# Optimization experiments

Hardware: AMD Instinct MI355X
Metric: run time of the kernel (lower is better)

## Reference

```python
import jax, jax.numpy as jnp
import numpy as np

B, S = 8, 512
HIDDEN = 513
SPATIAL = HIDDEN - 1           # 512
F = SPATIAL // 2 + 1           # 257 rfft bins
F2, F4 = 2 * F, 4 * F          # 514, 1028
IN_DIM = F2 + F2 + 2 * SPATIAL # 2052
MAX_STEPS = 20
TOL = 1e-3


def _ln(x, g, b):
    m = x.mean(-1, keepdims=True)
    v = ((x - m) ** 2).mean(-1, keepdims=True)
    return (x - m) * jax.lax.rsqrt(v + 1e-5) * g + b


def _freq_net(x, w1, b1, g, beta, w2, b2):
    # Linear -> LayerNorm -> GELU(exact) -> Linear -> Tanh
    h = jax.nn.gelu(_ln(x @ w1 + b1, g, beta), approximate=False)
    return jnp.tanh(h @ w2 + b2)


def _mlp(x, w1, b1, w2, b2):
    # Linear -> GELU(exact) -> Linear
    return jax.nn.gelu(x @ w1 + b1, approximate=False) @ w2 + b2


def setup_inputs() -> dict:
    key = jax.random.key(0)
    ks = jax.random.split(key, 16)
    def n(k, shape, s=0.05):
        return jax.random.normal(k, shape, jnp.float32) * s
    return dict(
        carrier_in=n(ks[0], (B, S, SPATIAL), 1.0),
        trajectory_in=n(ks[1], (B, S, SPATIAL), 1.0),
        source_pos=n(ks[2], (B, HIDDEN), 1.0),
        target_pos=n(ks[3], (B, HIDDEN), 1.0),
        cw1=n(ks[4], (IN_DIM, F4)), cb1=jnp.zeros(F4), cg=jnp.ones(F4), cbeta=jnp.zeros(F4),
        cw2=n(ks[5], (F4, F2)), cb2=jnp.zeros(F2),
        tw1=n(ks[6], (IN_DIM, F4)), tb1=jnp.zeros(F4), tg=jnp.ones(F4), tbeta=jnp.zeros(F4),
        tw2=n(ks[7], (F4, F2)), tb2=jnp.zeros(F2),
        freq_damping=jnp.linspace(0.95, 0.5, F).astype(jnp.float32),
        dw1=n(ks[8], (F2, F)), db1=jnp.zeros(F), dw2=n(ks[9], (F, 1)), db2=jnp.ones(1),
        sw1=n(ks[10], (F2, F // 2)), sb1=jnp.zeros(F // 2), sw2=n(ks[11], (F // 2, 1)), sb2=jnp.ones(1),
        carrier_scale=jnp.float32(0.1), trajectory_scale=jnp.float32(0.1),
    )


def reference(carrier_in, trajectory_in, source_pos, target_pos,
              cw1, cb1, cg, cbeta, cw2, cb2,
              tw1, tb1, tg, tbeta, tw2, tb2,
              freq_damping, dw1, db1, dw2, db2,
              sw1, sb1, sw2, sb2,
              carrier_scale, trajectory_scale):
    b, s, _ = carrier_in.shape
    src = jnp.broadcast_to(source_pos[:, None, :SPATIAL], (b, s, SPATIAL))
    tgt = jnp.broadcast_to(target_pos[:, None, :SPATIAL], (b, s, SPATIAL))

    def to_flat(x):  # rfft -> view_as_real -> flatten: [b,s,2F] (re,im interleaved)
        f = jnp.fft.rfft(x, axis=-1)
        return jnp.stack([f.real, f.imag], axis=-1).reshape(b, s, F2).astype(jnp.float32)

    c0 = to_flat(carrier_in)
    t0 = to_flat(trajectory_in)
    # torch: repeat(1,1,2).flatten -> tiled [d_0..d_{F-1}, d_0..d_{F-1}]
    damping = jnp.concatenate([freq_damping, freq_damping])

    def clamp10(x):
        nrm = jnp.linalg.norm(x)
        return jnp.where(nrm > 10.0, x * (10.0 / nrm), x)

    def step(carry, _):
        c, t, done = carry
        combined = jnp.concatenate([c, t, src, tgt], axis=-1)  # [b,s,IN_DIM]
        fc = _freq_net(combined, cw1, cb1, cg, cbeta, cw2, cb2)
        ft = _freq_net(combined, tw1, tb1, tg, tbeta, tw2, tb2)
        safe_c = jnp.nan_to_num(c, nan=0.0, posinf=1e6, neginf=-1e6)
        safe_t = jnp.nan_to_num(t, nan=0.0, posinf=1e6, neginf=-1e6)
        alpha_c = jax.nn.sigmoid(_mlp(safe_c, dw1, db1, dw2, db2))
        alpha_t = jax.nn.sigmoid(_mlp(safe_t, dw1, db1, dw2, db2))
        gamma = jax.nn.sigmoid(_mlp(safe_c, sw1, sb1, sw2, sb2)) + 0.5
        alpha_c = jnp.where(jnp.isnan(alpha_c), 0.0, alpha_c)
        alpha_t = jnp.where(jnp.isnan(alpha_t), 0.0, alpha_t)
        new_c = damping * c + gamma * alpha_c * carrier_scale * fc
        new_t = damping * t + gamma * alpha_t * trajectory_scale * ft
        dc = jnp.linalg.norm(new_c - c, axis=-1).mean()
        dt = jnp.linalg.norm(new_t - t, axis=-1).mean()
        conv = (dc < TOL) & (dt < TOL)
        # on convergence the torch loop breaks BEFORE the norm clamp
        out_c = jnp.where(conv, new_c, clamp10(new_c))
        out_t = jnp.where(conv, new_t, clamp10(new_t))
        out_c = jnp.where(done, c, out_c)
        out_t = jnp.where(done, t, out_t)
        return (out_c, out_t, done | conv), None

    (cf, tf, _), _ = jax.lax.scan(step, (c0, t0, jnp.array(False)), None, length=MAX_STEPS)

    def to_spatial(x):
        xr = x.reshape(b, s, F, 2)
        return jnp.fft.irfft(xr[..., 0] + 1j * xr[..., 1], n=SPATIAL, axis=-1).astype(jnp.float32)

    return to_spatial(cf), to_spatial(tf)


if __name__ == '__main__':
    out = reference(**setup_inputs())
    print(out[0].shape, out[1].shape)
```

## Files before the change

### kernel.cpp

```cpp
#include <hip/hip_runtime.h>
#include <hip/hip_bf16.h>
#include <math.h>

typedef __hip_bfloat16 bf16;
using s16x8 = __attribute__((ext_vector_type(8))) short;
using f32x4 = __attribute__((ext_vector_type(4))) float;
typedef __attribute__((address_space(1))) const unsigned int gu32;
typedef __attribute__((address_space(3))) unsigned int lu32;

#define RTOT 4096
#define XCT  1056
#define NT1  2304
#define HLD  2176
#define KH   1088
#define CLD  640
#define KDP  576
#define NDC  512
#define F2E  514
#define SP   512

__device__ __forceinline__ float gelu_ex(float x) {
    return 0.5f * x * (1.0f + erff(x * 0.70710678118654752f));
}
__device__ __forceinline__ float sigm(float x) { return 1.0f / (1.0f + expf(-x)); }
__device__ __forceinline__ float n2n(float x) {
    if (isnan(x)) return 0.0f;
    if (isinf(x)) return x > 0.0f ? 1e6f : -1e6f;
    return x;
}
__device__ __forceinline__ unsigned short bfb(float x) {
    __hip_bfloat16 h = __float2bfloat16(x);
    return *(unsigned short*)&h;
}
__device__ __forceinline__ unsigned packbf(float x, float y) {
    return (unsigned)bfb(x) | ((unsigned)bfb(y) << 16);
}
__device__ __forceinline__ void glds16(const bf16* g, short* l) {
    __builtin_amdgcn_global_load_lds((gu32*)g, (lu32*)l, 16, 0, 0);
}

template<int EPI>
__global__ __launch_bounds__(256)
void gemm_bt(const bf16* __restrict__ A, int lda,
             const bf16* __restrict__ Bt, int ldb,
             float* __restrict__ C, int ldc,
             const float* __restrict__ bias, int bias_ld, int ktiles,
             long zA, long zB, long zC, long zBias)
{
    A    += (long)blockIdx.z * zA;
    Bt   += (long)blockIdx.z * zB;
    C    += (long)blockIdx.z * zC;
    bias += (long)blockIdx.z * zBias;

    __shared__ __align__(16) short As[128 * 32];
    __shared__ __align__(16) short Bs[128 * 32];
    const int tid  = threadIdx.x;
    const int lane = tid & 63;
    const int wave = tid >> 6;
    const int l15  = lane & 15, kl = lane >> 4;
    const long mb = (long)blockIdx.x * 128;
    const long nb = (long)blockIdx.y * 128;
    const int wr = (wave >> 1) * 64;
    const int wc = (wave & 1) * 64;

    f32x4 acc[4][4] = {};

    const int grp_r = lane >> 2;
    const int gcol  = (lane & 3) * 8;
    const bf16* gA0 = A  + (mb + wave * 32 + grp_r) * (long)lda + gcol;
    const bf16* gA1 = gA0 + 16 * (long)lda;
    const bf16* gB0 = Bt + (nb + wave * 32 + grp_r) * (long)ldb + gcol;
    const bf16* gB1 = gB0 + 16 * (long)ldb;
    short* lA0 = &As[(wave * 32) * 32];
    short* lA1 = &As[(wave * 32 + 16) * 32];
    short* lB0 = &Bs[(wave * 32) * 32];
    short* lB1 = &Bs[(wave * 32 + 16) * 32];

    for (int kt = 0; kt < ktiles; ++kt) {
        const long ko = (long)kt * 32;
        __syncthreads();
        glds16(gA0 + ko, lA0);
        glds16(gA1 + ko, lA1);
        glds16(gB0 + ko, lB0);
        glds16(gB1 + ko, lB1);
        __syncthreads();
        s16x8 af[4], bfr[4];
#pragma unroll
        for (int m = 0; m < 4; ++m) {
            int ar = wr + m * 16 + l15;
            af[m] = *reinterpret_cast<const s16x8*>(&As[ar * 32 + kl * 8]);
        }
#pragma unroll
        for (int n = 0; n < 4; ++n) {
            int br = wc + n * 16 + l15;
            bfr[n] = *reinterpret_cast<const s16x8*>(&Bs[br * 32 + kl * 8]);
        }
#pragma unroll
        for (int m = 0; m < 4; ++m)
#pragma unroll
            for (int n = 0; n < 4; ++n)
                acc[m][n] = __builtin_amdgcn_mfma_f32_16x16x32_bf16(af[m], bfr[n], acc[m][n], 0, 0, 0);
    }

    const float* brow = bias + (bias_ld ? (long)(mb >> 9) * bias_ld : 0);
#pragma unroll
    for (int m = 0; m < 4; ++m) {
        const long grow0 = mb + wr + m * 16 + kl * 4;
#pragma unroll
        for (int n = 0; n < 4; ++n) {
            const long gcol2 = nb + wc + n * 16 + l15;
            const float bb = brow[gcol2];
            f32x4 v = acc[m][n];
#pragma unroll
            for (int r = 0; r < 4; ++r) {
                float x = v[r] + bb;
                if (EPI == 1) x = tanhf(x);
                else if (EPI == 2) x = gelu_ex(x);
                C[(grow0 + r) * (long)ldc + gcol2] = x;
            }
        }
    }
}

__global__ __launch_bounds__(256)
void sgemm_bt(const float* __restrict__ A, int lda,
              const float* __restrict__ Bt, int ldb,
              float* __restrict__ C, int ldc, int ktiles)
{
    __shared__ float As[16][68];
    __shared__ float Bs[16][68];
    const int tid = threadIdx.x;
    const int tx = tid & 15, ty = tid >> 4;
    const int lr = tid >> 2, lc = (tid & 3) * 4;
    const long mb = (long)blockIdx.x * 64, nb = (long)blockIdx.y * 64;
    float acc[4][4] = {};
    const float* Ap = A  + (mb + lr) * (long)lda + lc;
    const float* Bp = Bt + (nb + lr) * (long)ldb + lc;
    for (int kt = 0; kt < ktiles; ++kt) {
        float4 av = *(const float4*)(Ap + kt * 16);
        float4 bv = *(const float4*)(Bp + kt * 16);
        __syncthreads();
        As[lc + 0][lr] = av.x; As[lc + 1][lr] = av.y;
        As[lc + 2][lr] = av.z; As[lc + 3][lr] = av.w;
        Bs[lc + 0][lr] = bv.x; Bs[lc + 1][lr] = bv.y;
        Bs[lc + 2][lr] = bv.z; Bs[lc + 3][lr] = bv.w;
        __syncthreads();
#pragma unroll
        for (int kk = 0; kk < 16; ++kk) {
            float4 a = *(const float4*)&As[kk][ty * 4];
            float4 b = *(const float4*)&Bs[kk][tx * 4];
            acc[0][0] = fmaf(a.x, b.x, acc[0][0]); acc[0][1] = fmaf(a.x, b.y, acc[0][1]);
            acc[0][2] = fmaf(a.x, b.z, acc[0][2]); acc[0][3] = fmaf(a.x, b.w, acc[0][3]);
            acc[1][0] = fmaf(a.y, b.x, acc[1][0]); acc[1][1] = fmaf(a.y, b.y, acc[1][1]);
            acc[1][2] = fmaf(a.y, b.z, acc[1][2]); acc[1][3] = fmaf(a.y, b.w, acc[1][3]);
            acc[2][0] = fmaf(a.z, b.x, acc[2][0]); acc[2][1] = fmaf(a.z, b.y, acc[2][1]);
            acc[2][2] = fmaf(a.z, b.z, acc[2][2]); acc[2][3] = fmaf(a.z, b.w, acc[2][3]);
            acc[3][0] = fmaf(a.w, b.x, acc[3][0]); acc[3][1] = fmaf(a.w, b.y, acc[3][1]);
            acc[3][2] = fmaf(a.w, b.z, acc[3][2]); acc[3][3] = fmaf(a.w, b.w, acc[3][3]);
        }
    }
#pragma unroll
    for (int i = 0; i < 4; ++i) {
        float4 st = { acc[i][0], acc[i][1], acc[i][2], acc[i][3] };
        *(float4*)&C[(mb + ty * 4 + i) * (long)ldc + nb + tx * 4] = st;
    }
}

__global__ void build_tables(float* __restrict__ RT, float* __restrict__ IT)
{
    long idx = (long)blockIdx.x * 256 + threadIdx.x;
    const double W = 6.283185307179586476925286766559005768 / 512.0;
    if (idx < 640L * 512) {
        int r = (int)(idx >> 9), n = (int)(idx & 511);
        float v = 0.f;
        if (r < F2E) {
            int bin = r >> 1;
            int m = (bin * n) & 511;
            double ang = W * m;
            v = (r & 1) ? (float)(-sin(ang)) : (float)cos(ang);
        }
        RT[idx] = v;
    } else {
        long j2 = idx - 640L * 512;
        if (j2 < 512L * 640) {
            int n = (int)(j2 / 640), j = (int)(j2 % 640);
            float v = 0.f;
            if (j < F2E) {
                int bin = j >> 1;
                int m = (bin * n) & 511;
                double ang = W * m;
                bool edge = (bin == 0 || bin == 256);
                double ck = edge ? 1.0 : 2.0;
                if (j & 1) v = edge ? 0.f : (float)(-ck * sin(ang) / 512.0);
                else       v = (float)(ck * cos(ang) / 512.0);
            }
            IT[j2] = v;
        }
    }
}

__global__ void build_damp(float* damp, const float* __restrict__ fd)
{
    int i = blockIdx.x * 256 + threadIdx.x;
    if (i < F2E) damp[i] = fd[i < 257 ? i : i - 257];
}

__global__ void ybase_build(const float* __restrict__ srcp, const float* __restrict__ tgtp,
                            const float* __restrict__ cw1, const float* __restrict__ cb1,
                            const float* __restrict__ tw1, const float* __restrict__ tb1,
                            float* __restrict__ Yb)
{
    const int b = blockIdx.x;
    const int n = blockIdx.y * 256 + threadIdx.x;
    if (n >= NT1) return;
    float acc = 0.f;
    const bool isT = n >= 1152;
    const int nn = isT ? n - 1152 : n;
    if (nn < 1028) {
        const float* w  = isT ? tw1 : cw1;
        acc = (isT ? tb1 : cb1)[nn];
        const float* wst = w + (size_t)1028 * 1028 + nn;
        const float* wtg = w + (size_t)1540 * 1028 + nn;
        const float* s = srcp + b * 513;
        const float* t = tgtp + b * 513;
        for (int k = 0; k < 512; ++k) {
            acc = fmaf(s[k], wst[(size_t)k * 1028], acc);
            acc = fmaf(t[k], wtg[(size_t)k * 1028], acc);
        }
    }
    Yb[b * NT1 + n] = acc;
}

__global__ void wprep(bf16* __restrict__ dst, int ldk,
                      const float* s0, int K0, int N0, int r00,
                      const float* s1, int K1, int N1, int r01)
{
    int r = blockIdx.x;
    int k = blockIdx.y * 256 + threadIdx.x;
    if (k >= ldk) return;
    float v = 0.f;
    if (s0 && r >= r00 && r < r00 + N0 && k < K0) v = s0[(long)k * N0 + (r - r00)];
    if (s1 && r >= r01 && r < r01 + N1 && k < K1) v = s1[(long)k * N1 + (r - r01)];
    dst[(long)r * ldk + k] = __float2bfloat16(v);
}

__global__ void bias_fill(float* __restrict__ dst, int n,
                          const float* s0, int l0, int o0,
                          const float* s1, int l1, int o1)
{
    int i = blockIdx.x * 256 + threadIdx.x;
    if (i >= n) return;
    float v = 0.f;
    if (s0 && i >= o0 && i < o0 + l0) v = s0[i - o0];
    if (s1 && i >= o1 && i < o1 + l1) v = s1[i - o1];
    dst[i] = v;
}

__global__ void initconv(const float* __restrict__ cb, const float* __restrict__ tb,
                         bf16* __restrict__ X, bf16* __restrict__ Cb, bf16* __restrict__ Tb)
{
    int row = blockIdx.x;
    for (int j = threadIdx.x; j < F2E; j += 256) {
        float cv = cb[(long)row * CLD + j], tv = tb[(long)row * CLD + j];
        X[(long)row * XCT + j]        = __float2bfloat16(cv);
        X[(long)row * XCT + 514 + j]  = __float2bfloat16(tv);
        Cb[(long)row * KDP + j] = __float2bfloat16(n2n(cv));
        Tb[(long)row * KDP + j] = __float2bfloat16(n2n(tv));
    }
}

__global__ void xpad_zero(bf16* __restrict__ X)
{
    int row = blockIdx.x;
    int j = 1028 + threadIdx.x;
    if (j < XCT) X[(long)row * XCT + j] = __float2bfloat16(0.f);
}

__global__ __launch_bounds__(256)
void ln_gelu(const float* __restrict__ Y, bf16* __restrict__ H,
             const float* __restrict__ cg, const float* __restrict__ cbeta,
             const float* __restrict__ tg, const float* __restrict__ tbeta)
{
    const int lane = threadIdx.x & 63, wave = threadIdx.x >> 6;
    const int p = blockIdx.x * 4 + wave;
    const int row = p >> 1, net = p & 1;
    const float4* y4 = (const float4*)(Y + (long)row * NT1 + net * 1152);
    float4 v[4], vt = {0.f, 0.f, 0.f, 0.f};
    float s = 0.f;
#pragma unroll
    for (int k = 0; k < 4; ++k) {
        v[k] = y4[lane + k * 64];
        s += v[k].x + v[k].y + v[k].z + v[k].w;
    }
    if (lane == 0) { vt = y4[256]; s += vt.x + vt.y + vt.z + vt.w; }
#pragma unroll
    for (int o = 1; o < 64; o <<= 1) s += __shfl_xor(s, o, 64);
    const float mean = s * (1.0f / 1028.0f);
    float vs = 0.f;
#pragma unroll
    for (int k = 0; k < 4; ++k) {
        float a = v[k].x - mean, b = v[k].y - mean, c = v[k].z - mean, d = v[k].w - mean;
        vs += a * a + b * b + c * c + d * d;
    }
    if (lane == 0) {
        float a = vt.x - mean, b = vt.y - mean, c = vt.z - mean, d = vt.w - mean;
        vs += a * a + b * b + c * c + d * d;
    }
#pragma unroll
    for (int o = 1; o < 64; o <<= 1) vs += __shfl_xor(vs, o, 64);
    const float rs = rsqrtf(vs * (1.0f / 1028.0f) + 1e-5f);
    const float4* g4 = (const float4*)(net ? tg : cg);
    const float4* b4 = (const float4*)(net ? tbeta : cbeta);
    bf16* h = H + (long)row * HLD + (long)net * KH;
#pragma unroll
    for (int k = 0; k < 4; ++k) {
        int j = lane + k * 64;
        float4 gv = g4[j], bv = b4[j];
        ushort4 o;
        o.x = bfb(gelu_ex((v[k].x - mean) * rs * gv.x + bv.x));
        o.y = bfb(gelu_ex((v[k].y - mean) * rs * gv.y + bv.y));
        o.z = bfb(gelu_ex((v[k].z - mean) * rs * gv.z + bv.z));
        o.w = bfb(gelu_ex((v[k].w - mean) * rs * gv.w + bv.w));
        *(ushort4*)(&h[j * 4]) = o;
    }
    if (lane == 0) {
        float4 gv = g4[256], bv = b4[256];
        ushort4 o;
        o.x = bfb(gelu_ex((vt.x - mean) * rs * gv.x + bv.x));
        o.y = bfb(gelu_ex((vt.y - mean) * rs * gv.y + bv.y));
        o.z = bfb(gelu_ex((vt.z - mean) * rs * gv.z + bv.z));
        o.w = bfb(gelu_ex((vt.w - mean) * rs * gv.w + bv.w));
        *(ushort4*)(&h[1024]) = o;
    }
}

__global__ __launch_bounds__(256)
void fused_update(const float* __restrict__ Hd,
                  const float* __restrict__ dw2, const float* __restrict__ db2,
                  const float* __restrict__ sw2, const float* __restrict__ sb2,
                  const float* __restrict__ c, const float* __restrict__ t,
                  const float* __restrict__ fc, const float* __restrict__ ft,
                  float* __restrict__ nc, float* __restrict__ nt,
                  const float* __restrict__ damp,
                  const float* __restrict__ csc, const float* __restrict__ tsc,
                  float* __restrict__ part)
{
    __shared__ float red[16];
    const int tid = threadIdx.x, lane = tid & 63, wave = tid >> 6;
    const int row = blockIdx.x * 4 + wave;

    const float* hc = Hd + (long)row * NDC;
    const float* ht = Hd + (long)(4096 + row) * NDC;
    float s1 = 0.f, s2 = 0.f, s3 = 0.f;
#pragma unroll
    for (int k = 0; k < 4; ++k) {
        int j = lane + k * 64;
        s1 += hc[j] * dw2[j];
        s3 += ht[j] * dw2[j];
    }
    if (lane == 0) { s1 += hc[256] * dw2[256]; s3 += ht[256] * dw2[256]; }
#pragma unroll
    for (int k = 0; k < 2; ++k) {
        int j = lane + k * 64;
        s2 += hc[257 + j] * sw2[j];
    }
#pragma unroll
    for (int o = 1; o < 64; o <<= 1) {
        s1 += __shfl_xor(s1, o, 64);
        s2 += __shfl_xor(s2, o, 64);
        s3 += __shfl_xor(s3, o, 64);
    }
    float a  = sigm(s1 + db2[0]);
    float at = sigm(s3 + db2[0]);
    float g  = sigm(s2 + sb2[0]) + 0.5f;
    if (isnan(a))  a  = 0.f;
    if (isnan(at)) at = 0.f;
    const float gac = g * a  * csc[0];
    const float gat = g * at * tsc[0];

    const float2* c2  = (const float2*)(c  + (long)row * CLD);
    const float2* t2  = (const float2*)(t  + (long)row * CLD);
    const float2* fc2 = (const float2*)(fc + (long)row * CLD);
    const float2* ft2 = (const float2*)(ft + (long)row * CLD);
    float2* nc2 = (float2*)(nc + (long)row * CLD);
    float2* nt2 = (float2*)(nt + (long)row * CLD);
    const float2* d2 = (const float2*)damp;
    float sdc = 0.f, snc = 0.f, sdt = 0.f, snt = 0.f;
#pragma unroll
    for (int k = 0; k < 4; ++k) {
        int j = lane + k * 64;
        float2 dv = d2[j];
        float2 cv = c2[j], fv = fc2[j];
        float2 ncv = { dv.x * cv.x + gac * fv.x, dv.y * cv.y + gac * fv.y };
        nc2[j] = ncv;
        float dx = ncv.x - cv.x, dy = ncv.y - cv.y;
        sdc += dx * dx + dy * dy;
        snc += ncv.x * ncv.x + ncv.y * ncv.y;
        float2 tv = t2[j], gv = ft2[j];
        float2 ntv = { dv.x * tv.x + gat * gv.x, dv.y * tv.y + gat * gv.y };
        nt2[j] = ntv;
        dx = ntv.x - tv.x; dy = ntv.y - tv.y;
        sdt += dx * dx + dy * dy;
        snt += ntv.x * ntv.x + ntv.y * ntv.y;
    }
    if (lane == 0) {
        float2 dv = d2[256];
        float2 cv = c2[256], fv = fc2[256];
        float2 ncv = { dv.x * cv.x + gac * fv.x, dv.y * cv.y + gac * fv.y };
        nc2[256] = ncv;
        float dx = ncv.x - cv.x, dy = ncv.y - cv.y;
        sdc += dx * dx + dy * dy;
        snc += ncv.x * ncv.x + ncv.y * ncv.y;
        float2 tv = t2[256], gv = ft2[256];
        float2 ntv = { dv.x * tv.x + gat * gv.x, dv.y * tv.y + gat * gv.y };
        nt2[256] = ntv;
        dx = ntv.x - tv.x; dy = ntv.y - tv.y;
        sdt += dx * dx + dy * dy;
        snt += ntv.x * ntv.x + ntv.y * ntv.y;
    }
#pragma unroll
    for (int o = 1; o < 64; o <<= 1) {
        sdc += __shfl_xor(sdc, o, 64);
        snc += __shfl_xor(snc, o, 64);
        sdt += __shfl_xor(sdt, o, 64);
        snt += __shfl_xor(snt, o, 64);
    }
    if (lane == 0) {
        red[wave * 4 + 0] = sqrtf(sdc);
        red[wave * 4 + 1] = sqrtf(sdt);
        red[wave * 4 + 2] = snc;
        red[wave * 4 + 3] = snt;
    }
    __syncthreads();
    if (tid < 4)
        part[tid * 1024 + blockIdx.x] =
            red[0 * 4 + tid] + red[1 * 4 + tid] + red[2 * 4 + tid] + red[3 * 4 + tid];
}

__global__ __launch_bounds__(256)
void update2(const float* __restrict__ part, float* __restrict__ scal, int step)
{
    __shared__ float red[4];
    const int tid = threadIdx.x, lane = tid & 63, wave = tid >> 6;
    const float* pq = part + wave * 1024;
    float s = 0.f;
#pragma unroll
    for (int k = 0; k < 16; ++k) s += pq[lane + k * 64];
#pragma unroll
    for (int o = 1; o < 64; o <<= 1) s += __shfl_xor(s, o, 64);
    if (lane == 0) red[wave] = s;
    __syncthreads();
    if (tid == 0) {
        float dc = red[0] * (1.0f / 4096.0f);
        float dt = red[1] * (1.0f / 4096.0f);
        bool conv = (dc < 1e-3f) && (dt < 1e-3f);
        float done = scal[140];
        scal[120 + step] = (done != 0.f) ? 0.f : 1.f;
        float nrc = sqrtf(red[2]);
        float nrt = sqrtf(red[3]);
        scal[80 + step]  = conv ? 1.f : (nrc > 10.f ? 10.f / nrc : 1.f);
        scal[100 + step] = conv ? 1.f : (nrt > 10.f ? 10.f / nrt : 1.f);
        scal[140] = (done != 0.f || conv) ? 1.f : 0.f;
    }
}

__global__ __launch_bounds__(256)
void update3(float* __restrict__ c, float* __restrict__ t,
             const float* __restrict__ nc, const float* __restrict__ nt,
             bf16* __restrict__ X, bf16* __restrict__ Cb, bf16* __restrict__ Tb,
             const float* __restrict__ scal, int step)
{
    if (scal[120 + step] == 0.f) return;
    const float sc = scal[80 + step], st = scal[100 + step];
    const int lane = threadIdx.x & 63, wave = threadIdx.x >> 6;
    const int row = blockIdx.x * 4 + wave;
    const float2* nc2 = (const float2*)(nc + (long)row * CLD);
    const float2* nt2 = (const float2*)(nt + (long)row * CLD);
    float2* c2 = (float2*)(c + (long)row * CLD);
    float2* t2 = (float2*)(t + (long)row * CLD);
    bf16* xr = X  + (long)row * XCT;
    bf16* cb = Cb + (long)row * KDP;
    bf16* tb = Tb + (long)row * KDP;
#pragma unroll
    for (int k = 0; k < 5; ++k) {
        int j = lane + k * 64;
        if (k == 4 && lane > 0) break;
        float2 cv = nc2[j]; cv.x *= sc; cv.y *= sc;
        float2 tv = nt2[j]; tv.x *= st; tv.y *= st;
        c2[j] = cv;
        t2[j] = tv;
        *(unsigned*)(xr + j * 2)       = packbf(cv.x, cv.y);
        *(unsigned*)(xr + 514 + j * 2) = packbf(tv.x, tv.y);
        *(unsigned*)(cb + j * 2) = packbf(n2n(cv.x), n2n(cv.y));
        *(unsigned*)(tb + j * 2) = packbf(n2n(tv.x), n2n(tv.y));
    }
}

extern "C" void kernel_launch(void* const* d_in, const int* in_sizes, int n_in,
                              void* d_out, int out_size, void* d_ws, size_t ws_size,
                              hipStream_t stream)
{
    (void)in_sizes; (void)n_in; (void)out_size; (void)ws_size;
    const float* carrier = (const float*)d_in[0];
    const float* traj    = (const float*)d_in[1];
    const float* srcp    = (const float*)d_in[2];
    const float* tgtp    = (const float*)d_in[3];
    const float* cw1 = (const float*)d_in[4];  const float* cb1 = (const float*)d_in[5];
    const float* cg  = (const float*)d_in[6];  const float* cbe = (const float*)d_in[7];
    const float* cw2 = (const float*)d_in[8];  const float* cb2 = (const float*)d_in[9];
    const float* tw1 = (const float*)d_in[10]; const float* tb1 = (const float*)d_in[11];
    const float* tg  = (const float*)d_in[12]; const float* tbe = (const float*)d_in[13];
    const float* tw2 = (const float*)d_in[14]; const float* tb2 = (const float*)d_in[15];
    const float* fd  = (const float*)d_in[16];
    const float* dw1 = (const float*)d_in[17]; const float* db1 = (const float*)d_in[18];
    const float* dw2 = (const float*)d_in[19]; const float* db2 = (const float*)d_in[20];
    const float* sw1 = (const float*)d_in[21]; const float* sb1 = (const float*)d_in[22];
    const float* sw2 = (const float*)d_in[23]; const float* sb2 = (const float*)d_in[24];
    const float* csc = (const float*)d_in[25]; const float* tsc = (const float*)d_in[26];

    char* p = (char*)d_ws;
    size_t off = 0;
    auto take = [&](size_t bytes) { size_t o = off; off += (bytes + 255) & ~(size_t)255; return o; };
    bf16*  Xct  = (bf16*) (p + take((size_t)RTOT * XCT * 2));
    bf16*  W1ct = (bf16*) (p + take((size_t)NT1 * XCT * 2));
    float* Y    = (float*)(p + take((size_t)RTOT * NT1 * 4));
    bf16*  H    = (bf16*) (p + take((size_t)RTOT * HLD * 2));
    bf16*  W2t  = (bf16*) (p + take((size_t)1280 * KH * 2));
    bf16*  Wdc  = (bf16*) (p + take((size_t)NDC * KDP * 2));
    float* Ybase= (float*)(p + take((size_t)8 * NT1 * 4));
    float* b2c  = (float*)(p + take(1280 * 4));
    float* bdc  = (float*)(p + take(NDC * 4));
    float* RT   = (float*)(p + take(640L * 512 * 4));
    float* IT   = (float*)(p + take(512L * 640 * 4));
    float* damp = (float*)(p + take(F2E * 4));
    float* cbuf = (float*)(p + take((size_t)RTOT * CLD * 4));
    float* tbuf = (float*)(p + take((size_t)RTOT * CLD * 4));
    float* ncb  = (float*)(p + take((size_t)RTOT * CLD * 4));
    float* ntb  = (float*)(p + take((size_t)RTOT * CLD * 4));
    float* fcb  = (float*)(p + take((size_t)2 * RTOT * CLD * 4));
    float* ftb  = fcb + (size_t)RTOT * CLD;
    bf16*  Cbb  = (bf16*) (p + take((size_t)2 * RTOT * KDP * 2));
    bf16*  Tbb  = Cbb + (size_t)RTOT * KDP;
    float* Hd   = (float*)(p + take((size_t)2 * RTOT * NDC * 4));
    float* part = (float*)(p + take(4096 * 4));
    float* scal = (float*)(p + take(1024));

    hipMemsetAsync(scal, 0, 1024, stream);

    build_tables<<<2560, 256, 0, stream>>>(RT, IT);
    build_damp<<<3, 256, 0, stream>>>(damp, fd);
    ybase_build<<<dim3(8, 9), 256, 0, stream>>>(srcp, tgtp, cw1, cb1, tw1, tb1, Ybase);
    wprep<<<dim3(NT1, 5), 256, 0, stream>>>(W1ct, XCT, cw1, 1028, 1028, 0, tw1, 1028, 1028, 1152);
    wprep<<<dim3(1280, 5), 256, 0, stream>>>(W2t, KH, cw2, 1028, 514, 0, tw2, 1028, 514, 640);
    wprep<<<dim3(NDC, 3), 256, 0, stream>>>(Wdc, KDP, dw1, 514, 257, 0, sw1, 514, 128, 257);
    bias_fill<<<5, 256, 0, stream>>>(b2c, 1280, cb2, 514, 0, tb2, 514, 640);
    bias_fill<<<2, 256, 0, stream>>>(bdc, NDC, db1, 257, 0, sb1, 128, 257);
    xpad_zero<<<RTOT, 32, 0, stream>>>(Xct);

    sgemm_bt<<<dim3(64, 10), 256, 0, stream>>>(carrier, SP, RT, SP, cbuf, CLD, 32);
    sgemm_bt<<<dim3(64, 10), 256, 0, stream>>>(traj,    SP, RT, SP, tbuf, CLD, 32);
    initconv<<<RTOT, 256, 0, stream>>>(cbuf, tbuf, Xct, Cbb, Tbb);

    for (int s = 0; s < 20; ++s) {
        gemm_bt<0><<<dim3(32, 18), 256, 0, stream>>>(Xct, XCT, W1ct, XCT, Y, NT1,
                                                     Ybase, NT1, 33, 0, 0, 0, 0);
        ln_gelu<<<2048, 256, 0, stream>>>(Y, H, cg, cbe, tg, tbe);
        gemm_bt<1><<<dim3(32, 5, 2), 256, 0, stream>>>(H, HLD, W2t, KH, fcb, CLD,
                                                       b2c, 0, 34,
                                                       (long)KH, (long)640 * KH,
                                                       (long)RTOT * CLD, 640);
        gemm_bt<2><<<dim3(64, 4), 256, 0, stream>>>(Cbb, KDP, Wdc, KDP, Hd, NDC,
                                                    bdc, 0, 18, 0, 0, 0, 0);
        fused_update<<<1024, 256, 0, stream>>>(Hd, dw2, db2, sw2, sb2,
                                               cbuf, tbuf, fcb, ftb, ncb, ntb,
                                               damp, csc, tsc, part);
        update2<<<1, 256, 0, stream>>>(part, scal, s);
        update3<<<1024, 256, 0, stream>>>(cbuf, tbuf, ncb, ntb, Xct, Cbb, Tbb, scal, s);
    }

    float* out = (float*)d_out;
    sgemm_bt<<<dim3(64, 8), 256, 0, stream>>>(cbuf, CLD, IT, CLD, out, SP, 40);
    sgemm_bt<<<dim3(64, 8), 256, 0, stream>>>(tbuf, CLD, IT, CLD, out + (size_t)RTOT * SP, SP, 40);
}
```

Baseline: 3.141 ms.

## Pack first-layer output columns, split ybase reduction, fold convergence check into update

Packs the carrier and trajectory first-layer outputs contiguously (2176 columns instead of 2304 with padding), which removes one N-tile column from the per-step first GEMM grid. The ybase precompute is split across 16 K-slices plus a reduction kernel so the one-time setup has more parallelism. The single-block update2 kernel is removed: every update3 block now redundantly reduces the partial sums itself, saving one launch and one serial dependency per iteration. In exchange, each update3 block rereads 4096 partials, and the ln_gelu row offset of 1028 must stay aligned for float4 loads.

```diff
diff --git a/kernel.cpp b/kernel.cpp
--- a/kernel.cpp
+++ b/kernel.cpp
@@ -10,7 +10,7 @@
 
 #define RTOT 4096
 #define XCT  1056
-#define NT1  2304
+#define NT1  2176
 #define HLD  2176
 #define KH   1088
 #define CLD  640
@@ -18,6 +18,7 @@
 #define NDC  512
 #define F2E  514
 #define SP   512
+#define YZS  16
 
 __device__ __forceinline__ float gelu_ex(float x) {
     return 0.5f * x * (1.0f + erff(x * 0.70710678118654752f));
@@ -205,29 +206,39 @@
     if (i < F2E) damp[i] = fd[i < 257 ? i : i - 257];
 }
 
-__global__ void ybase_build(const float* __restrict__ srcp, const float* __restrict__ tgtp,
-                            const float* __restrict__ cw1, const float* __restrict__ cb1,
-                            const float* __restrict__ tw1, const float* __restrict__ tb1,
-                            float* __restrict__ Yb)
-{
-    const int b = blockIdx.x;
-    const int n = blockIdx.y * 256 + threadIdx.x;
+__global__ void ybase_part(const float* __restrict__ srcp, const float* __restrict__ tgtp,
+                           const float* __restrict__ cw1, const float* __restrict__ tw1,
+                           float* __restrict__ Yp)
+{
+    const int n = blockIdx.x * 256 + threadIdx.x;
+    const int b = blockIdx.y, z = blockIdx.z;
     if (n >= NT1) return;
     float acc = 0.f;
-    const bool isT = n >= 1152;
-    const int nn = isT ? n - 1152 : n;
-    if (nn < 1028) {
-        const float* w  = isT ? tw1 : cw1;
-        acc = (isT ? tb1 : cb1)[nn];
-        const float* wst = w + (size_t)1028 * 1028 + nn;
-        const float* wtg = w + (size_t)1540 * 1028 + nn;
+    if (n < 2056) {
+        const bool isT = (n >= 1028);
+        const int nn = isT ? n - 1028 : n;
+        const float* w = isT ? tw1 : cw1;
         const float* s = srcp + b * 513;
         const float* t = tgtp + b * 513;
-        for (int k = 0; k < 512; ++k) {
-            acc = fmaf(s[k], wst[(size_t)k * 1028], acc);
-            acc = fmaf(t[k], wtg[(size_t)k * 1028], acc);
-        }
-    }
+        const int k0 = z * (512 / YZS);
+        for (int k = k0; k < k0 + 512 / YZS; ++k) {
+            acc = fmaf(s[k], w[(size_t)(1028 + k) * 1028 + nn], acc);
+            acc = fmaf(t[k], w[(size_t)(1540 + k) * 1028 + nn], acc);
+        }
+    }
+    Yp[((size_t)z * 8 + b) * NT1 + n] = acc;
+}
+
+__global__ void ybase_reduce(const float* __restrict__ Yp,
+                             const float* __restrict__ cb1, const float* __restrict__ tb1,
+                             float* __restrict__ Yb)
+{
+    const int n = blockIdx.x * 256 + threadIdx.x;
+    const int b = blockIdx.y;
+    if (n >= NT1) return;
+    float acc = 0.f;
+    if (n < 2056) acc = (n < 1028) ? cb1[n] : tb1[n - 1028];
+    for (int z = 0; z < YZS; ++z) acc += Yp[((size_t)z * 8 + b) * NT1 + n];
     Yb[b * NT1 + n] = acc;
 }
 
@@ -284,7 +295,7 @@
     const int lane = threadIdx.x & 63, wave = threadIdx.x >> 6;
     const int p = blockIdx.x * 4 + wave;
     const int row = p >> 1, net = p & 1;
-    const float4* y4 = (const float4*)(Y + (long)row * NT1 + net * 1152);
+    const float4* y4 = (const float4*)(Y + (long)row * NT1 + net * 1028);
     float4 v[4], vt = {0.f, 0.f, 0.f, 0.f};
     float s = 0.f;
 #pragma unroll
@@ -438,41 +449,35 @@
 }
 
 __global__ __launch_bounds__(256)
-void update2(const float* __restrict__ part, float* __restrict__ scal, int step)
-{
-    __shared__ float red[4];
-    const int tid = threadIdx.x, lane = tid & 63, wave = tid >> 6;
-    const float* pq = part + wave * 1024;
-    float s = 0.f;
-#pragma unroll
-    for (int k = 0; k < 16; ++k) s += pq[lane + k * 64];
-#pragma unroll
-    for (int o = 1; o < 64; o <<= 1) s += __shfl_xor(s, o, 64);
-    if (lane == 0) red[wave] = s;
-    __syncthreads();
-    if (tid == 0) {
-        float dc = red[0] * (1.0f / 4096.0f);
-        float dt = red[1] * (1.0f / 4096.0f);
-        bool conv = (dc < 1e-3f) && (dt < 1e-3f);
-        float done = scal[140];
-        scal[120 + step] = (done != 0.f) ? 0.f : 1.f;
-        float nrc = sqrtf(red[2]);
-        float nrt = sqrtf(red[3]);
-        scal[80 + step]  = conv ? 1.f : (nrc > 10.f ? 10.f / nrc : 1.f);
-        scal[100 + step] = conv ? 1.f : (nrt > 10.f ? 10.f / nrt : 1.f);
-        scal[140] = (done != 0.f || conv) ? 1.f : 0.f;
-    }
-}
-
-__global__ __launch_bounds__(256)
 void update3(float* __restrict__ c, float* __restrict__ t,
              const float* __restrict__ nc, const float* __restrict__ nt,
              bf16* __restrict__ X, bf16* __restrict__ Cb, bf16* __restrict__ Tb,
-             const float* __restrict__ scal, int step)
-{
-    if (scal[120 + step] == 0.f) return;
-    const float sc = scal[80 + step], st = scal[100 + step];
-    const int lane = threadIdx.x & 63, wave = threadIdx.x >> 6;
+             const float* __restrict__ part, float* __restrict__ scal, int step)
+{
+    __shared__ float red[4];
+    const int tid = threadIdx.x, lane = tid & 63, wave = tid >> 6;
+    {
+        const float* pq = part + wave * 1024;
+        float s = 0.f;
+#pragma unroll
+        for (int k = 0; k < 16; ++k) s += pq[lane + k * 64];
+#pragma unroll
+        for (int o = 1; o < 64; o <<= 1) s += __shfl_xor(s, o, 64);
+        if (lane == 0) red[wave] = s;
+    }
+    __syncthreads();
+    const float done = scal[step];
+    const float dc = red[0] * (1.0f / 4096.0f);
+    const float dt = red[1] * (1.0f / 4096.0f);
+    const bool conv = (dc < 1e-3f) && (dt < 1e-3f);
+    if (blockIdx.x == 0 && tid == 0)
+        scal[step + 1] = (done != 0.f || conv) ? 1.f : 0.f;
+    if (done != 0.f) return;
+    const float nrc = sqrtf(red[2]);
+    const float nrt = sqrtf(red[3]);
+    const float sc = conv ? 1.f : (nrc > 10.f ? 10.f / nrc : 1.f);
+    const float st = conv ? 1.f : (nrt > 10.f ? 10.f / nrt : 1.f);
+
     const int row = blockIdx.x * 4 + wave;
     const float2* nc2 = (const float2*)(nc + (long)row * CLD);
     const float2* nt2 = (const float2*)(nt + (long)row * CLD);
@@ -528,6 +533,7 @@
     bf16*  W2t  = (bf16*) (p + take((size_t)1280 * KH * 2));
     bf16*  Wdc  = (bf16*) (p + take((size_t)NDC * KDP * 2));
     float* Ybase= (float*)(p + take((size_t)8 * NT1 * 4));
+    float* Ypart= (float*)(p + take((size_t)YZS * 8 * NT1 * 4));
     float* b2c  = (float*)(p + take(1280 * 4));
     float* bdc  = (float*)(p + take(NDC * 4));
     float* RT   = (float*)(p + take(640L * 512 * 4));
@@ -549,8 +555,9 @@
 
     build_tables<<<2560, 256, 0, stream>>>(RT, IT);
     build_damp<<<3, 256, 0, stream>>>(damp, fd);
-    ybase_build<<<dim3(8, 9), 256, 0, stream>>>(srcp, tgtp, cw1, cb1, tw1, tb1, Ybase);
-    wprep<<<dim3(NT1, 5), 256, 0, stream>>>(W1ct, XCT, cw1, 1028, 1028, 0, tw1, 1028, 1028, 1152);
+    ybase_part<<<dim3(9, 8, YZS), 256, 0, stream>>>(srcp, tgtp, cw1, tw1, Ypart);
+    ybase_reduce<<<dim3(9, 8), 256, 0, stream>>>(Ypart, cb1, tb1, Ybase);
+    wprep<<<dim3(NT1, 5), 256, 0, stream>>>(W1ct, XCT, cw1, 1028, 1028, 0, tw1, 1028, 1028, 1028);
     wprep<<<dim3(1280, 5), 256, 0, stream>>>(W2t, KH, cw2, 1028, 514, 0, tw2, 1028, 514, 640);
     wprep<<<dim3(NDC, 3), 256, 0, stream>>>(Wdc, KDP, dw1, 514, 257, 0, sw1, 514, 128, 257);
     bias_fill<<<5, 256, 0, stream>>>(b2c, 1280, cb2, 514, 0, tb2, 514, 640);
@@ -562,7 +569,7 @@
     initconv<<<RTOT, 256, 0, stream>>>(cbuf, tbuf, Xct, Cbb, Tbb);
 
     for (int s = 0; s < 20; ++s) {
-        gemm_bt<0><<<dim3(32, 18), 256, 0, stream>>>(Xct, XCT, W1ct, XCT, Y, NT1,
+        gemm_bt<0><<<dim3(32, 17), 256, 0, stream>>>(Xct, XCT, W1ct, XCT, Y, NT1,
                                                      Ybase, NT1, 33, 0, 0, 0, 0);
         ln_gelu<<<2048, 256, 0, stream>>>(Y, H, cg, cbe, tg, tbe);
         gemm_bt<1><<<dim3(32, 5, 2), 256, 0, stream>>>(H, HLD, W2t, KH, fcb, CLD,
@@ -574,8 +581,8 @@
         fused_update<<<1024, 256, 0, stream>>>(Hd, dw2, db2, sw2, sb2,
                                                cbuf, tbuf, fcb, ftb, ncb, ntb,
                                                damp, csc, tsc, part);
-        update2<<<1, 256, 0, stream>>>(part, scal, s);
-        update3<<<1024, 256, 0, stream>>>(cbuf, tbuf, ncb, ntb, Xct, Cbb, Tbb, scal, s);
+        update3<<<1024, 256, 0, stream>>>(cbuf, tbuf, ncb, ntb, Xct, Cbb, Tbb,
+                                          part, scal, s);
     }
 
     float* out = (float*)d_out;
```

Measured after the change: 3.133 ms. No clear change (-0.2%).
